# Kernel tuning notes

Measured on AMD Instinct MI355X. Metric: run time of the kernel, lower is better.

## Reference

```python
import math
import jax, jax.numpy as jnp
import numpy as np

B, S, D, H, V, NZ = 2, 2048, 1024, 16, 4096, 10
DK = D // H
KAPPA = 1.0
GAMMA_VALS = [14.1347, 21.022, 25.0109, 30.4249, 32.9351,
              37.5862, 40.9187, 43.3271, 48.0052, 49.7738]


def setup_inputs() -> dict:
    key = jax.random.key(0)
    ks = jax.random.split(key, 12)
    w_scale = 1.0 / math.sqrt(D)
    x = jax.random.normal(ks[0], (B, S, D), dtype=jnp.float32)
    wq = jax.random.normal(ks[1], (D, D), dtype=jnp.float32) * w_scale
    wk = jax.random.normal(ks[2], (D, D), dtype=jnp.float32) * w_scale
    wv = jax.random.normal(ks[3], (D, D), dtype=jnp.float32) * w_scale
    wo = jax.random.normal(ks[4], (D, D), dtype=jnp.float32) * w_scale
    bq = jax.random.normal(ks[5], (D,), dtype=jnp.float32) * 0.01
    bk = jax.random.normal(ks[6], (D,), dtype=jnp.float32) * 0.01
    bv = jax.random.normal(ks[7], (D,), dtype=jnp.float32) * 0.01
    bo = jax.random.normal(ks[8], (D,), dtype=jnp.float32) * 0.01
    semantic_token_ids = jax.random.randint(ks[9], (B, S), 0, V)
    # constitutional charter mask: mostly-allowed boolean (stored as float buffer)
    omega_mask = (jax.random.uniform(ks[10], (V, V)) < 0.95).astype(jnp.float32)
    causal_mask = jnp.tril(jnp.ones((S, S), dtype=bool))
    gamma = jnp.asarray(GAMMA_VALS[:NZ], dtype=jnp.float32)
    return {
        "x": x, "wq": wq, "bq": bq, "wk": wk, "bk": bk,
        "wv": wv, "bv": bv, "wo": wo, "bo": bo,
        "omega_mask": omega_mask, "gamma": gamma,
        "semantic_token_ids": semantic_token_ids, "causal_mask": causal_mask,
    }


def _memory_kernel(seq_len, gamma):
    idx = jnp.arange(seq_len, dtype=jnp.float32)
    delta = jnp.abs(idx[:, None] - idx[None, :])            # [S, S]
    decay = jnp.exp(-KAPPA * delta)
    log_delta = jnp.log(delta + 1.0)
    cos_sum = jnp.sum(jnp.cos(gamma[:, None, None] * log_delta[None]), axis=0)
    return decay * cos_sum                                   # [S, S]


def reference(x, wq, bq, wk, bk, wv, bv, wo, bo,
              omega_mask, gamma, semantic_token_ids, causal_mask):
    batch, seq_len, _ = x.shape
    q = (x @ wq.T + bq).reshape(batch, seq_len, H, DK)
    k = (x @ wk.T + bk).reshape(batch, seq_len, H, DK)
    v = (x @ wv.T + bv).reshape(batch, seq_len, H, DK)
    scores = jnp.einsum('bihd,bjhd->bhij', q, k) / math.sqrt(DK)  # [B,H,S,S]
    M = _memory_kernel(seq_len, gamma)                            # [S,S]
    scores = scores * M[None, None]
    # seq_omega[b,i,j] = omega_mask[ids[b,i], ids[b,j]]
    ids = semantic_token_ids
    seq_omega = omega_mask[ids[:, :, None], ids[:, None, :]]      # [B,S,S]
    scores = jnp.where(seq_omega[:, None] == 0, -1e9, scores)
    scores = jnp.where(causal_mask[None, None], scores, -1e9)
    attn = jax.nn.softmax(scores, axis=-1)
    out = jnp.einsum('bhij,bjhd->bihd', attn, v).reshape(batch, seq_len, D)
    return out @ wo.T + bo
```

## Files before the change

### kernel.cpp

```cpp
#include <hip/hip_runtime.h>
#include <math.h>
#include <float.h>

#define B_ 2
#define S_ 2048
#define D_ 1024
#define H_ 16
#define V_ 4096
#define NZ_ 10
#define BS_ (B_ * S_)

typedef __attribute__((ext_vector_type(8))) __bf16 bf16x8;
typedef __attribute__((ext_vector_type(4))) float f32x4;
typedef unsigned long long ull;

#define MFMA16(a, b, c) __builtin_amdgcn_mfma_f32_16x16x32_bf16((a), (b), (c), 0, 0, 0)

__device__ __forceinline__ unsigned short f2bf(float f) {
  unsigned u = __builtin_bit_cast(unsigned, f);
  u = (u + 0x7FFFu + ((u >> 16) & 1u)) >> 16;
  return (unsigned short)u;
}
__device__ __forceinline__ float bf2f(unsigned short h) {
  unsigned u = ((unsigned)h) << 16;
  return __builtin_bit_cast(float, u);
}

__global__ __launch_bounds__(256) void prep_kernel(
    const float* __restrict__ x,
    const float* __restrict__ wq, const float* __restrict__ wk,
    const float* __restrict__ wv, const float* __restrict__ wo,
    const float* __restrict__ omega, const float* __restrict__ gamma,
    unsigned short* __restrict__ xh, unsigned short* __restrict__ xl,
    unsigned short* __restrict__ wqh, unsigned short* __restrict__ wql,
    unsigned short* __restrict__ wkh, unsigned short* __restrict__ wkl,
    unsigned short* __restrict__ wvh, unsigned short* __restrict__ woh,
    ull* __restrict__ obit, float* __restrict__ mbg) {
  const int bid = blockIdx.x;
  const int t = threadIdx.x;
  if (bid < 4096) {
    int i = (bid * 256 + t) * 4;
    float4 v = *(const float4*)(x + i);
    ushort4 h;
    h.x = f2bf(v.x); h.y = f2bf(v.y); h.z = f2bf(v.z); h.w = f2bf(v.w);
    *(ushort4*)(xh + i) = h;
    ushort4 l;
    l.x = f2bf(v.x - bf2f(h.x));
    l.y = f2bf(v.y - bf2f(h.y));
    l.z = f2bf(v.z - bf2f(h.z));
    l.w = f2bf(v.w - bf2f(h.w));
    *(ushort4*)(xl + i) = l;
  } else if (bid < 8192) {
    int idx = ((bid - 4096) * 256 + t) * 4;
    int w = idx >> 20;
    int off = idx & ((1 << 20) - 1);
    const float* src; unsigned short* hi; unsigned short* lo;
    if (w == 0)      { src = wq; hi = wqh; lo = wql; }
    else if (w == 1) { src = wk; hi = wkh; lo = wkl; }
    else if (w == 2) { src = wv; hi = wvh; lo = nullptr; }
    else             { src = wo; hi = woh; lo = nullptr; }
    float4 v = *(const float4*)(src + off);
    ushort4 h;
    h.x = f2bf(v.x); h.y = f2bf(v.y); h.z = f2bf(v.z); h.w = f2bf(v.w);
    *(ushort4*)(hi + off) = h;
    if (lo) {
      ushort4 l;
      l.x = f2bf(v.x - bf2f(h.x));
      l.y = f2bf(v.y - bf2f(h.y));
      l.z = f2bf(v.z - bf2f(h.z));
      l.w = f2bf(v.w - bf2f(h.w));
      *(ushort4*)(lo + off) = l;
    }
  } else if (bid < 8192 + 4096) {
    int base = (bid - 8192) * 4096;
#pragma unroll
    for (int c = 0; c < 16; ++c) {
      int e = base + c * 256 + t;
      bool ok = omega[e] != 0.f;
      ull mask = __ballot(ok);
      if ((t & 63) == 0) obit[e >> 6] = mask;
    }
  } else {
    if (t < 64) {
      float delta = (float)t;
      float ld = logf(delta + 1.f);
      float cs = 0.f;
#pragma unroll
      for (int z = 0; z < NZ_; ++z) cs += cosf(gamma[z] * ld);
      mbg[t] = expf(-delta) * cs * 0.125f;
    }
  }
}

__global__ __launch_bounds__(256) void maskbits_kernel(const int* __restrict__ ids,
                                                       const ull* __restrict__ obit,
                                                       ull* __restrict__ fmask,
                                                       int* __restrict__ c0,
                                                       ull* __restrict__ bm) {
  const int grow = blockIdx.x;
  const int b = grow >> 11, i = grow & 2047;
  const int t = threadIdx.x, lane = t & 63, wave = t >> 6;
  const int idi = ids[grow];
  const ull* orow = obit + ((size_t)idi << 6);
  __shared__ int cnt;
  if (t == 0) cnt = 0;
  if (t < 64) {
    int jj = i - t;
    bool ok = false;
    if (jj >= 0) {
      int idj = ids[b * S_ + jj];
      ok = (orow[idj >> 6] >> (idj & 63)) & 1ull;
    }
    ull mask = __ballot(ok);
    if (t == 0) bm[grow] = mask;
  }
  __syncthreads();
  const int jmax = i - 64;
  int pc = 0;
#pragma unroll
  for (int c = 0; c < 8; ++c) {
    int j = c * 256 + t;
    bool on = false;
    if (j <= jmax) {
      int idj = ids[b * S_ + j];
      on = (orow[idj >> 6] >> (idj & 63)) & 1ull;
    }
    ull mk = __ballot(on);
    if (lane == 0) {
      fmask[(size_t)grow * 32 + c * 4 + wave] = mk;
      pc += (int)__popcll(mk);
    }
  }
  if (lane == 0 && pc) atomicAdd(&cnt, pc);
  __syncthreads();
  if (t == 0) c0[grow] = cnt;
}

template <int NT>
__device__ __forceinline__ void stage_tiles(const unsigned short* const* gb,
                                            int wave, int lane, int K, int k0,
                                            unsigned short* dst) {
#pragma unroll
  for (int tile = 0; tile < NT; ++tile) {
#pragma unroll
    for (int half = 0; half < 2; ++half) {
      int c = wave + half * 4;
      int s = (c << 6) + lane;
      int row = s >> 2;
      int cq = (s & 3) ^ ((s >> 3) & 3);
      const unsigned short* g = gb[tile] + (size_t)row * K + k0 + (cq << 3);
      unsigned short* l = dst + tile * 4096 + (s << 3);
      __builtin_amdgcn_global_load_lds((const __attribute__((address_space(1))) void*)g,
                                       (__attribute__((address_space(3))) void*)l,
                                       16, 0, 0);
    }
  }
}

__device__ __forceinline__ void frag_loads(const unsigned short* tb, int base, int wsel,
                                           int m, int quad, bf16x8 (&f)[4]) {
#pragma unroll
  for (int i = 0; i < 4; ++i) {
    int r = wsel * 64 + i * 16 + m;
    f[i] = *(const bf16x8*)&tb[base + r * 32 + ((quad ^ ((r >> 1) & 3)) << 3)];
  }
}

__device__ __forceinline__ void qkv_compute(const unsigned short* tb, bool split,
                                            int wm, int wn, int m, int quad,
                                            f32x4 (&acc)[4][4]) {
  bf16x8 afh[4], bfh[4];
  frag_loads(tb, 0 * 4096, wm, m, quad, afh);
  frag_loads(tb, 1 * 4096, wn, m, quad, bfh);
  if (split) {
    bf16x8 afl[4], bfl[4];
    frag_loads(tb, 2 * 4096, wm, m, quad, afl);
    frag_loads(tb, 3 * 4096, wn, m, quad, bfl);
#pragma unroll
    for (int mt = 0; mt < 4; ++mt)
#pragma unroll
      for (int nt = 0; nt < 4; ++nt) {
        acc[mt][nt] = MFMA16(afh[mt], bfh[nt], acc[mt][nt]);
        acc[mt][nt] = MFMA16(afl[mt], bfh[nt], acc[mt][nt]);
        acc[mt][nt] = MFMA16(afh[mt], bfl[nt], acc[mt][nt]);
      }
  } else {
#pragma unroll
    for (int mt = 0; mt < 4; ++mt)
#pragma unroll
      for (int nt = 0; nt < 4; ++nt)
        acc[mt][nt] = MFMA16(afh[mt], bfh[nt], acc[mt][nt]);
  }
}

__global__ __launch_bounds__(256) void mfma_gemm_qkv(
    const unsigned short* __restrict__ xh, const unsigned short* __restrict__ xl,
    const unsigned short* __restrict__ wqh, const unsigned short* __restrict__ wql,
    const unsigned short* __restrict__ wkh, const unsigned short* __restrict__ wkl,
    const unsigned short* __restrict__ wvh,
    const float* __restrict__ bq, const float* __restrict__ bk,
    const float* __restrict__ bv,
    unsigned short* __restrict__ qoh, unsigned short* __restrict__ qol,
    unsigned short* __restrict__ koh, unsigned short* __restrict__ kol,
    unsigned short* __restrict__ vt) {
  __shared__ unsigned short tiles[2][4 * 4096];
  const int t = threadIdx.x;
  const int wave = t >> 6, lane = t & 63;
  const int which = blockIdx.x >> 3;
  const int n0 = (blockIdx.x & 7) * 128;
  const int i0 = blockIdx.y * 128;
  const int K = D_, N = D_;
  const int wm = wave >> 1, wn = wave & 1;
  const int m = lane & 15, quad = lane >> 4;

  const unsigned short* Wh = (which == 0) ? wqh : (which == 1) ? wkh : wvh;
  const unsigned short* Wl = (which == 0) ? wql : wkl;
  const float* bias = (which == 0) ? bq : (which == 1) ? bk : bv;
  unsigned short* Chi = (which == 0) ? qoh : (which == 1) ? koh : vt;
  unsigned short* Clo = (which == 0) ? qol : (which == 1) ? kol : nullptr;
  const bool split = (which < 2);

  const unsigned short* gb[4];
  gb[0] = xh + (size_t)i0 * K;
  gb[1] = Wh + (size_t)n0 * K;
  gb[2] = xl + (size_t)i0 * K;
  gb[3] = Wl + (size_t)n0 * K;

  f32x4 acc[4][4] = {};

  if (split) stage_tiles<4>(gb, wave, lane, K, 0, tiles[0]);
  else       stage_tiles<2>(gb, wave, lane, K, 0, tiles[0]);
  __syncthreads();

  for (int k0 = 0; k0 < K; k0 += 64) {
    if (split) stage_tiles<4>(gb, wave, lane, K, k0 + 32, tiles[1]);
    else       stage_tiles<2>(gb, wave, lane, K, k0 + 32, tiles[1]);
    qkv_compute(tiles[0], split, wm, wn, m, quad, acc);
    __syncthreads();
    if (k0 + 64 < K) {
      if (split) stage_tiles<4>(gb, wave, lane, K, k0 + 64, tiles[0]);
      else       stage_tiles<2>(gb, wave, lane, K, k0 + 64, tiles[0]);
    }
    qkv_compute(tiles[1], split, wm, wn, m, quad, acc);
    __syncthreads();
  }

  float bvv[4];
#pragma unroll
  for (int nt = 0; nt < 4; ++nt) bvv[nt] = bias[n0 + wn * 64 + nt * 16 + m];

  if (which == 2) {
    unsigned short* E = &tiles[0][0];
#pragma unroll
    for (int mt = 0; mt < 4; ++mt)
#pragma unroll
      for (int nt = 0; nt < 4; ++nt) {
        int lc = wn * 64 + nt * 16 + m;
#pragma unroll
        for (int r = 0; r < 4; ++r) {
          int lr = wm * 64 + mt * 16 + quad * 4 + r;
          E[lr * 132 + lc] = f2bf(acc[mt][nt][r] + bvv[nt]);
        }
      }
    __syncthreads();
    const int bq2 = i0 >> 11, il0 = i0 & 2047;
    for (int c = t; c < 4096; c += 256) {
      int lcol = c >> 5, i4 = (c & 31) << 2;
      ushort4 vv;
      vv.x = E[(i4 + 0) * 132 + lcol];
      vv.y = E[(i4 + 1) * 132 + lcol];
      vv.z = E[(i4 + 2) * 132 + lcol];
      vv.w = E[(i4 + 3) * 132 + lcol];
      *(ushort4*)(Chi + ((size_t)bq2 * D_ + n0 + lcol) * S_ + il0 + i4) = vv;
    }
  } else {
#pragma unroll
    for (int mt = 0; mt < 4; ++mt) {
      int rbase = i0 + wm * 64 + mt * 16 + quad * 4;
#pragma unroll
      for (int nt = 0; nt < 4; ++nt) {
        int col = n0 + wn * 64 + nt * 16 + m;
#pragma unroll
        for (int r = 0; r < 4; ++r) {
          float val = acc[mt][nt][r] + bvv[nt];
          size_t idx = (size_t)(rbase + r) * N + col;
          unsigned short hv = f2bf(val);
          Chi[idx] = hv;
          Clo[idx] = f2bf(val - bf2f(hv));
        }
      }
    }
  }
}

__global__ __launch_bounds__(256) void mfma_gemm_o(const unsigned short* __restrict__ Ah,
                                                   const unsigned short* __restrict__ Wh,
                                                   const float* __restrict__ bias,
                                                   float* __restrict__ C,
                                                   int M, int N, int K) {
  __shared__ unsigned short tiles[2][2 * 4096];
  const int t = threadIdx.x;
  const int wave = t >> 6, lane = t & 63;
  const int i0 = blockIdx.y * 128, n0 = blockIdx.x * 128;
  const int wm = wave >> 1, wn = wave & 1;
  const int m = lane & 15, quad = lane >> 4;

  const unsigned short* gb[2];
  gb[0] = Ah + (size_t)i0 * K;
  gb[1] = Wh + (size_t)n0 * K;

  f32x4 acc[4][4] = {};

  stage_tiles<2>(gb, wave, lane, K, 0, tiles[0]);
  __syncthreads();

  for (int k0 = 0; k0 < K; k0 += 64) {
    stage_tiles<2>(gb, wave, lane, K, k0 + 32, tiles[1]);
    qkv_compute(tiles[0], false, wm, wn, m, quad, acc);
    __syncthreads();
    if (k0 + 64 < K) stage_tiles<2>(gb, wave, lane, K, k0 + 64, tiles[0]);
    qkv_compute(tiles[1], false, wm, wn, m, quad, acc);
    __syncthreads();
  }

  float bvv[4];
#pragma unroll
  for (int nt = 0; nt < 4; ++nt) bvv[nt] = bias[n0 + wn * 64 + nt * 16 + m];
#pragma unroll
  for (int mt = 0; mt < 4; ++mt) {
    int rbase = i0 + wm * 64 + mt * 16 + quad * 4;
#pragma unroll
    for (int nt = 0; nt < 4; ++nt) {
      int col = n0 + wn * 64 + nt * 16 + m;
#pragma unroll
      for (int r = 0; r < 4; ++r)
        C[(size_t)(rbase + r) * N + col] = acc[mt][nt][r] + bvv[nt];
    }
  }
}

__global__ __launch_bounds__(256) void vsum_kernel(const unsigned short* __restrict__ vt,
                                                   float* __restrict__ vsum) {
  const int t = threadIdx.x;
  const int dg = blockIdx.x * 64 + (t >> 2);
  const int k = t & 3;
  const unsigned short* p = vt + (size_t)dg * S_;
  float s = 0.f;
  for (int c = 0; c < 64; ++c) {
    int j = (c * 4 + k) * 8;
    ushort4 a = *(const ushort4*)(p + j);
    ushort4 b4 = *(const ushort4*)(p + j + 4);
    s += bf2f(a.x) + bf2f(a.y) + bf2f(a.z) + bf2f(a.w) +
         bf2f(b4.x) + bf2f(b4.y) + bf2f(b4.z) + bf2f(b4.w);
  }
  s += __shfl_xor(s, 1);
  s += __shfl_xor(s, 2);
  if (k == 0) vsum[dg] = s;
}

__device__ __forceinline__ void t64_stageB(const unsigned short* __restrict__ Bb,
                                           int wave, int lane, int strideB, int k0,
                                           unsigned short* dstB) {
#pragma unroll
  for (int half = 0; half < 2; ++half) {
    int c = wave + half * 4;
    int s = (c << 6) + lane;
    int row = s >> 2;
    int cq = (s & 3) ^ ((s >> 3) & 3);
    const unsigned short* g = Bb + (size_t)row * strideB + k0 + (cq << 3);
    __builtin_amdgcn_global_load_lds((const __attribute__((address_space(1))) void*)g,
                                     (__attribute__((address_space(3))) void*)(dstB + (s << 3)),
                                     16, 0, 0);
  }
}

__device__ __forceinline__ void t64_compute(const unsigned short* tb,
                                            int wm, int wn, int m, int quad,
                                            f32x4 (&acc)[2][4]) {
  bf16x8 af[2], bf[4];
#pragma unroll
  for (int i = 0; i < 2; ++i) {
    int r = wm * 32 + i * 16 + m;
    af[i] = *(const bf16x8*)&tb[r * 32 + ((quad ^ ((r >> 1) & 3)) << 3)];
  }
#pragma unroll
  for (int i = 0; i < 4; ++i) {
    int r = wn * 64 + i * 16 + m;
    bf[i] = *(const bf16x8*)&tb[2048 + r * 32 + ((quad ^ ((r >> 1) & 3)) << 3)];
  }
#pragma unroll
  for (int mt = 0; mt < 2; ++mt)
#pragma unroll
    for (int nt = 0; nt < 4; ++nt)
      acc[mt][nt] = MFMA16(af[mt], bf[nt], acc[mt][nt]);
}

__device__ __forceinline__ void fs_buildA(const ull* __restrict__ fm0, int t, int k0,
                                          unsigned short* dstA) {
  int row = t >> 2, q = t & 3;
  int cq = q ^ ((row >> 1) & 3);
  int kb = k0 + (cq << 3);
  ull w = fm0[(size_t)row * 32 + (kb >> 6)];
  unsigned byte = (unsigned)(w >> (kb & 63)) & 0xFFu;
  uint4 v;
  v.x = ((byte & 1u)   ? 0x3F80u : 0u) | ((byte & 2u)   ? 0x3F800000u : 0u);
  v.y = ((byte & 4u)   ? 0x3F80u : 0u) | ((byte & 8u)   ? 0x3F800000u : 0u);
  v.z = ((byte & 16u)  ? 0x3F80u : 0u) | ((byte & 32u)  ? 0x3F800000u : 0u);
  v.w = ((byte & 64u)  ? 0x3F80u : 0u) | ((byte & 128u) ? 0x3F800000u : 0u);
  *(uint4*)&dstA[t << 3] = v;
}

__global__ __launch_bounds__(256) void farsum_gemm(const unsigned short* __restrict__ vt,
                                                   const ull* __restrict__ fmask,
                                                   unsigned short* __restrict__ fsum) {
  __shared__ unsigned short ft[2][6144];
  const int t = threadIdx.x, wave = t >> 6, lane = t & 63;
  const int m = lane & 15, quad = lane >> 4;
  const int wm = wave >> 1, wn = wave & 1;
  const int n0 = blockIdx.x * 128;
  const int y = blockIdx.y, half = y >> 5, u = y & 31;
  const int b = u & 1;
  const int q = half ? (u >> 1) : (31 - (u >> 1));
  const int il0 = q * 64;
  const int grow0 = b * S_ + il0;
  const unsigned short* Bb = vt + ((size_t)b * D_ + n0) * S_;
  const ull* fm0 = fmask + (size_t)grow0 * 32;
  const int kend = il0;

  f32x4 acc[2][4] = {};
  if (kend > 0) {
    t64_stageB(Bb, wave, lane, S_, 0, &ft[0][2048]);
    fs_buildA(fm0, t, 0, &ft[0][0]);
    __syncthreads();
    for (int k0 = 0; k0 < kend; k0 += 64) {
      t64_stageB(Bb, wave, lane, S_, k0 + 32, &ft[1][2048]);
      fs_buildA(fm0, t, k0 + 32, &ft[1][0]);
      t64_compute(&ft[0][0], wm, wn, m, quad, acc);
      __syncthreads();
      if (k0 + 64 < kend) {
        t64_stageB(Bb, wave, lane, S_, k0 + 64, &ft[0][2048]);
        fs_buildA(fm0, t, k0 + 64, &ft[0][0]);
      }
      t64_compute(&ft[1][0], wm, wn, m, quad, acc);
      __syncthreads();
    }
  }
#pragma unroll
  for (int mt = 0; mt < 2; ++mt)
#pragma unroll
    for (int nt = 0; nt < 4; ++nt) {
      int col = n0 + wn * 64 + nt * 16 + m;
#pragma unroll
      for (int r = 0; r < 4; ++r) {
        int row = grow0 + wm * 32 + mt * 16 + quad * 4 + r;
        fsum[(size_t)row * D_ + col] = f2bf(acc[mt][nt][r]);
      }
    }
}

__global__ __launch_bounds__(256, 3) void attn4_kernel(
    const unsigned short* __restrict__ qh, const unsigned short* __restrict__ ql,
    const unsigned short* __restrict__ kh, const unsigned short* __restrict__ kl,
    const unsigned short* __restrict__ vt, const unsigned short* __restrict__ farsum,
    const int* __restrict__ c0arr, const float* __restrict__ vsum,
    const ull* __restrict__ bm, const float* __restrict__ mbg,
    unsigned short* __restrict__ out) {
  const int h = blockIdx.x, i0 = blockIdx.y * 64, b = blockIdx.z;
  const int jt0 = i0 - 64;
  __shared__ unsigned short Qhs[64 * 72];
  __shared__ unsigned short Khs[128 * 72];
  __shared__ unsigned short Vt[64 * 136];
  __shared__ float mrow[64], lrow[64], Mband[64];
  __shared__ float rmaxw[4][32], rsumw[4][32];
  __shared__ ull bmr[64];
  __shared__ int c0r[64];
  const int t = threadIdx.x, lane = t & 63, wave = t >> 6;
  const int m = lane & 15, quad = lane >> 4;
  const int wm = wave >> 1, wn = wave & 1;

  bf16x8 aL[2][2], bL[4][2];
#pragma unroll
  for (int mt = 0; mt < 2; ++mt)
#pragma unroll
    for (int kc = 0; kc < 2; ++kc) {
      int row = i0 + wm * 32 + mt * 16 + m;
      aL[mt][kc] = *(const bf16x8*)(ql + ((size_t)(b * S_) + row) * D_ + h * 64 + kc * 32 + quad * 8);
    }
#pragma unroll
  for (int nt = 0; nt < 4; ++nt)
#pragma unroll
    for (int kc = 0; kc < 2; ++kc) {
      int jr = jt0 + wn * 64 + nt * 16 + m;
      if (jr < 0) jr = 0;
      bL[nt][kc] = *(const bf16x8*)(kl + ((size_t)(b * S_) + jr) * D_ + h * 64 + kc * 32 + quad * 8);
    }

  for (int c = t; c < 1024; c += 256) {
    int r = c >> 4, d4 = (c & 15) << 2;
    size_t g = ((size_t)(b * S_) + i0 + r) * D_ + h * 64 + d4;
    *(ushort4*)&Qhs[r * 72 + d4] = *(const ushort4*)(qh + g);
  }
  for (int c = t; c < 2048; c += 256) {
    int r = c >> 4, d4 = (c & 15) << 2;
    int jr = jt0 + r;
    if (jr < 0) jr = 0;
    size_t g = ((size_t)(b * S_) + jr) * D_ + h * 64 + d4;
    *(ushort4*)&Khs[r * 72 + d4] = *(const ushort4*)(kh + g);
  }
  for (int c = t; c < 2048; c += 256) {
    int d = c >> 5, j4 = (c & 31) << 2;
    int j = jt0 + j4;
    if (j < 0) j = 0;
    *(ushort4*)&Vt[d * 136 + j4] =
        *(const ushort4*)(vt + ((size_t)(b * D_) + h * 64 + d) * S_ + j);
  }
  if (t < 64) {
    Mband[t] = mbg[t];
    int grow = b * S_ + i0 + t;
    bmr[t] = bm[grow];
    int c0v = c0arr[grow];
    c0r[t] = c0v;
    mrow[t] = (c0v > 0) ? 0.f : -FLT_MAX;
  }
  __syncthreads();

  f32x4 accS[2][4] = {};
#pragma unroll
  for (int kc = 0; kc < 2; ++kc) {
    bf16x8 aH[2], bH[4];
#pragma unroll
    for (int mt = 0; mt < 2; ++mt)
      aH[mt] = *(const bf16x8*)&Qhs[(wm * 32 + mt * 16 + m) * 72 + kc * 32 + quad * 8];
#pragma unroll
    for (int nt = 0; nt < 4; ++nt)
      bH[nt] = *(const bf16x8*)&Khs[(wn * 64 + nt * 16 + m) * 72 + kc * 32 + quad * 8];
#pragma unroll
    for (int mt = 0; mt < 2; ++mt)
#pragma unroll
      for (int nt = 0; nt < 4; ++nt) {
        accS[mt][nt] = MFMA16(aH[mt], bH[nt], accS[mt][nt]);
        accS[mt][nt] = MFMA16(aL[mt][kc], bH[nt], accS[mt][nt]);
        accS[mt][nt] = MFMA16(aH[mt], bL[nt][kc], accS[mt][nt]);
      }
  }

  float rmx[2][4];
#pragma unroll
  for (int mt = 0; mt < 2; ++mt)
#pragma unroll
    for (int r = 0; r < 4; ++r) rmx[mt][r] = -FLT_MAX;
#pragma unroll
  for (int mt = 0; mt < 2; ++mt)
#pragma unroll
    for (int nt = 0; nt < 4; ++nt)
#pragma unroll
      for (int r = 0; r < 4; ++r) {
        int il = wm * 32 + mt * 16 + quad * 4 + r;
        int jl = wn * 64 + nt * 16 + m;
        int dlt = il + 64 - jl;
        float s = -FLT_MAX;
        if (dlt >= 0 && dlt < 64 && ((bmr[il] >> dlt) & 1ull))
          s = accS[mt][nt][r] * Mband[dlt];
        accS[mt][nt][r] = s;
        rmx[mt][r] = fmaxf(rmx[mt][r], s);
      }
#pragma unroll
  for (int off = 1; off < 16; off <<= 1)
#pragma unroll
    for (int mt = 0; mt < 2; ++mt)
#pragma unroll
      for (int r = 0; r < 4; ++r)
        rmx[mt][r] = fmaxf(rmx[mt][r], __shfl_xor(rmx[mt][r], off));
  if (m == 0)
#pragma unroll
    for (int mt = 0; mt < 2; ++mt)
#pragma unroll
      for (int r = 0; r < 4; ++r)
        rmaxw[wave][mt * 16 + quad * 4 + r] = rmx[mt][r];
  __syncthreads();
  if (t < 64) {
    int wmw = t >> 5, idx = t & 31;
    float tmax = fmaxf(rmaxw[wmw * 2][idx], rmaxw[wmw * 2 + 1][idx]);
    mrow[t] = fmaxf(mrow[t], tmax);
  }
  __syncthreads();

  unsigned short* Pl = Khs;
  float rs[2][4] = {};
#pragma unroll
  for (int mt = 0; mt < 2; ++mt)
#pragma unroll
    for (int nt = 0; nt < 4; ++nt)
#pragma unroll
      for (int r = 0; r < 4; ++r) {
        int il = wm * 32 + mt * 16 + quad * 4 + r;
        int jl = wn * 64 + nt * 16 + m;
        float s = accS[mt][nt][r];
        float p = (s > -1e37f) ? expf(s - mrow[il]) : 0.f;
        rs[mt][r] += p;
        Pl[il * 136 + jl] = f2bf(p);
      }
#pragma unroll
  for (int off = 1; off < 16; off <<= 1)
#pragma unroll
    for (int mt = 0; mt < 2; ++mt)
#pragma unroll
      for (int r = 0; r < 4; ++r)
        rs[mt][r] += __shfl_xor(rs[mt][r], off);
  if (m == 0)
#pragma unroll
    for (int mt = 0; mt < 2; ++mt)
#pragma unroll
      for (int r = 0; r < 4; ++r)
        rsumw[wave][mt * 16 + quad * 4 + r] = rs[mt][r];
  __syncthreads();
  if (t < 64) {
    int wmw = t >> 5, idx = t & 31;
    lrow[t] = rsumw[wmw * 2][idx] + rsumw[wmw * 2 + 1][idx];
  }

  f32x4 accO[2][2] = {};
#pragma unroll
  for (int kc = 0; kc < 4; ++kc) {
    bf16x8 aP[2], bV[2];
#pragma unroll
    for (int mt = 0; mt < 2; ++mt)
      aP[mt] = *(const bf16x8*)&Pl[(wm * 32 + mt * 16 + m) * 136 + kc * 32 + quad * 8];
#pragma unroll
    for (int nt = 0; nt < 2; ++nt)
      bV[nt] = *(const bf16x8*)&Vt[(wn * 32 + nt * 16 + m) * 136 + kc * 32 + quad * 8];
#pragma unroll
    for (int mt = 0; mt < 2; ++mt)
#pragma unroll
      for (int nt = 0; nt < 2; ++nt)
        accO[mt][nt] = MFMA16(aP[mt], bV[nt], accO[mt][nt]);
  }
  __syncthreads();

#pragma unroll
  for (int mt = 0; mt < 2; ++mt)
#pragma unroll
    for (int r = 0; r < 4; ++r) {
      int il = wm * 32 + mt * 16 + quad * 4 + r;
      int gi = i0 + il;
      float mv = mrow[il], l = lrow[il];
      int C0 = c0r[il];
      float efar = (C0 > 0) ? expf(-mv) : 0.f;
      float denom = l + (float)C0 * efar;
      bool degen = (l == 0.f && C0 == 0);
      if (degen) denom = (float)S_;
      float inv = 1.f / denom;
#pragma unroll
      for (int nt = 0; nt < 2; ++nt) {
        int d = wn * 32 + nt * 16 + m;
        size_t base = ((size_t)(b * S_) + gi) * D_ + h * 64 + d;
        float o = accO[mt][nt][r];
        if (C0 > 0) o += efar * bf2f(farsum[base]);
        if (degen) o = vsum[b * D_ + h * 64 + d];
        out[base] = f2bf(o * inv);
      }
    }
}

extern "C" void kernel_launch(void* const* d_in, const int* in_sizes, int n_in,
                              void* d_out, int out_size, void* d_ws, size_t ws_size,
                              hipStream_t stream) {
  const float* x     = (const float*)d_in[0];
  const float* wq    = (const float*)d_in[1];
  const float* bq    = (const float*)d_in[2];
  const float* wk    = (const float*)d_in[3];
  const float* bk    = (const float*)d_in[4];
  const float* wv    = (const float*)d_in[5];
  const float* bv    = (const float*)d_in[6];
  const float* wo    = (const float*)d_in[7];
  const float* bo    = (const float*)d_in[8];
  const float* omega = (const float*)d_in[9];
  const float* gamma = (const float*)d_in[10];
  const int*   ids   = (const int*)d_in[11];
  float* out = (float*)d_out;

  char* ws = (char*)d_ws;
  const size_t SZH = (size_t)BS_ * D_ * 2;
  const size_t WH  = (size_t)D_ * D_ * 2;
  unsigned short* qhb = (unsigned short*)(ws);
  unsigned short* qlb = (unsigned short*)(ws + 1 * SZH);
  unsigned short* khb = (unsigned short*)(ws + 2 * SZH);
  unsigned short* klb = (unsigned short*)(ws + 3 * SZH);
  unsigned short* vtb = (unsigned short*)(ws + 4 * SZH);
  unsigned short* xl    = (unsigned short*)(ws + 5 * SZH);
  unsigned short* fsumh = xl;
  unsigned short* xh    = (unsigned short*)(ws + 6 * SZH);
  unsigned short* ah    = xh;
  char* wp = ws + 7 * SZH;
  unsigned short* wqh = (unsigned short*)(wp);
  unsigned short* wql = (unsigned short*)(wp + 1 * WH);
  unsigned short* wkh = (unsigned short*)(wp + 2 * WH);
  unsigned short* wkl = (unsigned short*)(wp + 3 * WH);
  unsigned short* wvh = (unsigned short*)(wp + 4 * WH);
  unsigned short* woh = (unsigned short*)(wp + 5 * WH);
  char* tail = wp + 6 * WH;
  ull* obit = (ull*)tail;
  float* vsumf = (float*)(tail + (size_t)V_ * 64 * 8);
  int* c0 = (int*)((char*)vsumf + (size_t)B_ * D_ * 4);
  ull* bmask = (ull*)((char*)c0 + (size_t)BS_ * 4);
  float* mbg = (float*)((char*)bmask + (size_t)BS_ * 8);
  ull* fmask = (ull*)((char*)mbg + 256);

  prep_kernel<<<8192 + 4096 + 1, 256, 0, stream>>>(
      x, wq, wk, wv, wo, omega, gamma,
      xh, xl, wqh, wql, wkh, wkl, wvh, woh, obit, mbg);

  maskbits_kernel<<<BS_, 256, 0, stream>>>(ids, obit, fmask, c0, bmask);

  mfma_gemm_qkv<<<dim3(24, 32), 256, 0, stream>>>(xh, xl, wqh, wql, wkh, wkl, wvh,
                                                  bq, bk, bv, qhb, qlb, khb, klb, vtb);

  vsum_kernel<<<(B_ * D_) / 64, 256, 0, stream>>>(vtb, vsumf);

  farsum_gemm<<<dim3(D_ / 128, 64), 256, 0, stream>>>(vtb, fmask, fsumh);

  attn4_kernel<<<dim3(H_, S_ / 64, B_), 256, 0, stream>>>(qhb, qlb, khb, klb, vtb, fsumh, c0,
                                                          vsumf, bmask, mbg, ah);

  mfma_gemm_o<<<dim3(D_ / 128, BS_ / 128), 256, 0, stream>>>(ah, woh, bo, out, BS_, D_, D_);
}
```

Before: 350.3 us.

## Merge maskbits into QKV GEMM grid and vsum into farsum grid

The standalone maskbits kernel is folded into the QKV GEMM launch as extra grid rows (blockIdx.y >= 32), reusing the GEMM's shared memory for the counter. The vsum reduction is folded into farsum_gemm as an extra grid row, with one thread per output summing a whole row serially. This removes two kernel launches and lets the independent mask work overlap with GEMM blocks. The serial per-thread vsum loop gives less memory parallelism and may become a tail on the farsum launch.

Result: no change. 350.7 us, median of 2 (+0.1%).

```diff
diff --git a/kernel.cpp b/kernel.cpp
--- a/kernel.cpp
+++ b/kernel.cpp
@@ -92,50 +92,6 @@
   }
 }
 
-__global__ __launch_bounds__(256) void maskbits_kernel(const int* __restrict__ ids,
-                                                       const ull* __restrict__ obit,
-                                                       ull* __restrict__ fmask,
-                                                       int* __restrict__ c0,
-                                                       ull* __restrict__ bm) {
-  const int grow = blockIdx.x;
-  const int b = grow >> 11, i = grow & 2047;
-  const int t = threadIdx.x, lane = t & 63, wave = t >> 6;
-  const int idi = ids[grow];
-  const ull* orow = obit + ((size_t)idi << 6);
-  __shared__ int cnt;
-  if (t == 0) cnt = 0;
-  if (t < 64) {
-    int jj = i - t;
-    bool ok = false;
-    if (jj >= 0) {
-      int idj = ids[b * S_ + jj];
-      ok = (orow[idj >> 6] >> (idj & 63)) & 1ull;
-    }
-    ull mask = __ballot(ok);
-    if (t == 0) bm[grow] = mask;
-  }
-  __syncthreads();
-  const int jmax = i - 64;
-  int pc = 0;
-#pragma unroll
-  for (int c = 0; c < 8; ++c) {
-    int j = c * 256 + t;
-    bool on = false;
-    if (j <= jmax) {
-      int idj = ids[b * S_ + j];
-      on = (orow[idj >> 6] >> (idj & 63)) & 1ull;
-    }
-    ull mk = __ballot(on);
-    if (lane == 0) {
-      fmask[(size_t)grow * 32 + c * 4 + wave] = mk;
-      pc += (int)__popcll(mk);
-    }
-  }
-  if (lane == 0 && pc) atomicAdd(&cnt, pc);
-  __syncthreads();
-  if (t == 0) c0[grow] = cnt;
-}
-
 template <int NT>
 __device__ __forceinline__ void stage_tiles(const unsigned short* const* gb,
                                             int wave, int lane, int K, int k0,
@@ -202,10 +158,54 @@
     const float* __restrict__ bv,
     unsigned short* __restrict__ qoh, unsigned short* __restrict__ qol,
     unsigned short* __restrict__ koh, unsigned short* __restrict__ kol,
-    unsigned short* __restrict__ vt) {
+    unsigned short* __restrict__ vt,
+    const int* __restrict__ ids, const ull* __restrict__ obit,
+    ull* __restrict__ fmask, int* __restrict__ c0, ull* __restrict__ bm) {
   __shared__ unsigned short tiles[2][4 * 4096];
   const int t = threadIdx.x;
   const int wave = t >> 6, lane = t & 63;
+
+  if (blockIdx.y >= 32) {
+    int grow = (blockIdx.y - 32) * 24 + blockIdx.x;
+    if (grow >= BS_) return;
+    const int b = grow >> 11, i = grow & 2047;
+    const int idi = ids[grow];
+    const ull* orow = obit + ((size_t)idi << 6);
+    int* cntp = (int*)&tiles[0][0];
+    if (t == 0) *cntp = 0;
+    if (t < 64) {
+      int jj = i - t;
+      bool ok = false;
+      if (jj >= 0) {
+        int idj = ids[b * S_ + jj];
+        ok = (orow[idj >> 6] >> (idj & 63)) & 1ull;
+      }
+      ull mask = __ballot(ok);
+      if (t == 0) bm[grow] = mask;
+    }
+    __syncthreads();
+    const int jmax = i - 64;
+    int pc = 0;
+#pragma unroll
+    for (int c = 0; c < 8; ++c) {
+      int j = c * 256 + t;
+      bool on = false;
+      if (j <= jmax) {
+        int idj = ids[b * S_ + j];
+        on = (orow[idj >> 6] >> (idj & 63)) & 1ull;
+      }
+      ull mk = __ballot(on);
+      if (lane == 0) {
+        fmask[(size_t)grow * 32 + c * 4 + wave] = mk;
+        pc += (int)__popcll(mk);
+      }
+    }
+    if (lane == 0 && pc) atomicAdd(cntp, pc);
+    __syncthreads();
+    if (t == 0) c0[grow] = *cntp;
+    return;
+  }
+
   const int which = blockIdx.x >> 3;
   const int n0 = (blockIdx.x & 7) * 128;
   const int i0 = blockIdx.y * 128;
@@ -337,25 +337,6 @@
         C[(size_t)(rbase + r) * N + col] = acc[mt][nt][r] + bvv[nt];
     }
   }
-}
-
-__global__ __launch_bounds__(256) void vsum_kernel(const unsigned short* __restrict__ vt,
-                                                   float* __restrict__ vsum) {
-  const int t = threadIdx.x;
-  const int dg = blockIdx.x * 64 + (t >> 2);
-  const int k = t & 3;
-  const unsigned short* p = vt + (size_t)dg * S_;
-  float s = 0.f;
-  for (int c = 0; c < 64; ++c) {
-    int j = (c * 4 + k) * 8;
-    ushort4 a = *(const ushort4*)(p + j);
-    ushort4 b4 = *(const ushort4*)(p + j + 4);
-    s += bf2f(a.x) + bf2f(a.y) + bf2f(a.z) + bf2f(a.w) +
-         bf2f(b4.x) + bf2f(b4.y) + bf2f(b4.z) + bf2f(b4.w);
-  }
-  s += __shfl_xor(s, 1);
-  s += __shfl_xor(s, 2);
-  if (k == 0) vsum[dg] = s;
 }
 
 __device__ __forceinline__ void t64_stageB(const unsigned short* __restrict__ Bb,
@@ -412,9 +393,25 @@
 
 __global__ __launch_bounds__(256) void farsum_gemm(const unsigned short* __restrict__ vt,
                                                    const ull* __restrict__ fmask,
-                                                   unsigned short* __restrict__ fsum) {
+                                                   unsigned short* __restrict__ fsum,
+                                                   float* __restrict__ vsum) {
   __shared__ unsigned short ft[2][6144];
   const int t = threadIdx.x, wave = t >> 6, lane = t & 63;
+
+  if (blockIdx.y == 64) {
+    int dg = blockIdx.x * 256 + t;
+    const unsigned short* p = vt + (size_t)dg * S_;
+    float s = 0.f;
+    for (int c = 0; c < 256; ++c) {
+      ushort4 a = *(const ushort4*)(p + c * 8);
+      ushort4 b4 = *(const ushort4*)(p + c * 8 + 4);
+      s += bf2f(a.x) + bf2f(a.y) + bf2f(a.z) + bf2f(a.w) +
+           bf2f(b4.x) + bf2f(b4.y) + bf2f(b4.z) + bf2f(b4.w);
+    }
+    vsum[dg] = s;
+    return;
+  }
+
   const int m = lane & 15, quad = lane >> 4;
   const int wm = wave >> 1, wn = wave & 1;
   const int n0 = blockIdx.x * 128;
@@ -710,14 +707,11 @@
       x, wq, wk, wv, wo, omega, gamma,
       xh, xl, wqh, wql, wkh, wkl, wvh, woh, obit, mbg);
 
-  maskbits_kernel<<<BS_, 256, 0, stream>>>(ids, obit, fmask, c0, bmask);
-
-  mfma_gemm_qkv<<<dim3(24, 32), 256, 0, stream>>>(xh, xl, wqh, wql, wkh, wkl, wvh,
-                                                  bq, bk, bv, qhb, qlb, khb, klb, vtb);
-
-  vsum_kernel<<<(B_ * D_) / 64, 256, 0, stream>>>(vtb, vsumf);
-
-  farsum_gemm<<<dim3(D_ / 128, 64), 256, 0, stream>>>(vtb, fmask, fsumh);
+  mfma_gemm_qkv<<<dim3(24, 32 + 171), 256, 0, stream>>>(
+      xh, xl, wqh, wql, wkh, wkl, wvh, bq, bk, bv,
+      qhb, qlb, khb, klb, vtb, ids, obit, fmask, c0, bmask);
+
+  farsum_gemm<<<dim3(D_ / 128, 65), 256, 0, stream>>>(vtb, fmask, fsumh, vsumf);
 
   attn4_kernel<<<dim3(H_, S_ / 64, B_), 256, 0, stream>>>(qhb, qlb, khb, klb, vtb, fsumh, c0,
                                                           vsumf, bmask, mbg, ah);
```
